# Kernel tuning notes

Hardware: AMD Instinct MI355X
Metric: run time of the kernel (lower is better)

The kernel has to match this reference:

```python
import jax, jax.numpy as jnp
import numpy as np

N_NODES = 50000
N_EDGES = 600000
D_IN = 128
D_HID = 128
NUM_LAYERS = 4


def setup_inputs() -> dict:
    key = jax.random.key(0)
    ks = jax.random.split(key, 8)
    x = jax.random.normal(ks[0], (N_NODES, D_IN), dtype=jnp.float32)
    edge_index = jax.random.randint(ks[1], (2, N_EDGES), 0, N_NODES, dtype=jnp.int32)
    s = 0.05
    # first_conv: lin_rel (weight+bias) applied to aggregated neighbors, lin_root (no bias) applied to x
    W1 = jax.random.normal(ks[2], (D_IN, D_HID), dtype=jnp.float32) * s
    b1 = jnp.zeros((D_HID,), dtype=jnp.float32)
    R1 = jax.random.normal(ks[3], (D_IN, D_HID), dtype=jnp.float32) * s
    # shared conv used for layers 2..NUM_LAYERS
    W2 = jax.random.normal(ks[4], (D_HID, D_HID), dtype=jnp.float32) * s
    b2 = jnp.zeros((D_HID,), dtype=jnp.float32)
    R2 = jax.random.normal(ks[5], (D_HID, D_HID), dtype=jnp.float32) * s
    return {"x": x, "edge_index": edge_index, "W1": W1, "b1": b1, "R1": R1,
            "W2": W2, "b2": b2, "R2": R2}


def _graph_conv(x, src, dst, W, b, R, num_nodes):
    # gather source features, scatter-max into destinations (PyG GraphConv, aggr='max')
    agg = jax.ops.segment_max(x[src], dst, num_segments=num_nodes)  # [N, d]
    agg = jnp.where(jnp.isneginf(agg), 0.0, agg)  # isolated nodes -> 0 (PyG fill)
    return agg @ W + b + x @ R  # lin_rel(agg) + lin_root(x)


def reference(x, edge_index, W1, b1, R1, W2, b2, R2):
    src, dst = edge_index[0], edge_index[1]
    n = x.shape[0]
    h = jax.nn.relu(_graph_conv(x, src, dst, W1, b1, R1, n))
    for _ in range(NUM_LAYERS - 1):  # shared weights, per original module
        h = jax.nn.relu(_graph_conv(h, src, dst, W2, b2, R2, n))
    return h
```

## Files before the change

kernel.cpp:

```cpp
#include <hip/hip_runtime.h>
#include <math.h>

static constexpr int NNODES = 50000;
static constexpr int NEDGES = 600000;
static constexpr int D = 128;
static constexpr int NPART = (NNODES + 255) / 256;

typedef __attribute__((ext_vector_type(8))) short short8;
typedef __attribute__((ext_vector_type(4))) float f32x4;

static __device__ inline unsigned short f2bf_rne(float f) {
  unsigned u = __float_as_uint(f);
  unsigned r = (u + 0x7FFFu + ((u >> 16) & 1u)) >> 16;
  return (unsigned short)r;
}
static __device__ inline float bf2f(unsigned short s) {
  return __uint_as_float(((unsigned)s) << 16);
}

__global__ __launch_bounds__(256) void split_kernel(const float* __restrict__ x,
    unsigned short* __restrict__ hi, unsigned short* __restrict__ lo, int n4) {
  int i = blockIdx.x * 256 + threadIdx.x;
  if (i >= n4) return;
  f32x4 v = *(const f32x4*)(x + (size_t)i * 4);
  ushort4 h, l;
  h.x = f2bf_rne(v[0]); l.x = f2bf_rne(v[0] - bf2f(h.x));
  h.y = f2bf_rne(v[1]); l.y = f2bf_rne(v[1] - bf2f(h.y));
  h.z = f2bf_rne(v[2]); l.z = f2bf_rne(v[2] - bf2f(h.z));
  h.w = f2bf_rne(v[3]); l.w = f2bf_rne(v[3] - bf2f(h.w));
  *(ushort4*)(hi + (size_t)i * 4) = h;
  *(ushort4*)(lo + (size_t)i * 4) = l;
}


__global__ void count_kernel(const int* __restrict__ dst, int* __restrict__ cnt, int nE) {
  int i = blockIdx.x * blockDim.x + threadIdx.x;
  if (i < nE) atomicAdd(&cnt[dst[i]], 1);
}

__global__ void scan_partial(const int* __restrict__ cnt, int* __restrict__ part, int n) {
  int i = blockIdx.x * 256 + threadIdx.x;
  int v = (i < n) ? cnt[i] : 0;
#pragma unroll
  for (int off = 32; off > 0; off >>= 1) v += __shfl_down(v, off);
  __shared__ int ws[4];
  int wid = threadIdx.x >> 6, lane = threadIdx.x & 63;
  if (lane == 0) ws[wid] = v;
  __syncthreads();
  if (threadIdx.x == 0) part[blockIdx.x] = ws[0] + ws[1] + ws[2] + ws[3];
}

__global__ void scan_root(const int* __restrict__ part, int* __restrict__ pscan,
                          int* __restrict__ rs_last, int np) {
  int i = threadIdx.x;
  int v = (i < np) ? part[i] : 0;
  int incl = v;
  int lane = i & 63, wid = i >> 6;
#pragma unroll
  for (int off = 1; off < 64; off <<= 1) {
    int t = __shfl_up(incl, off);
    if (lane >= off) incl += t;
  }
  __shared__ int ws[4];
  if (lane == 63) ws[wid] = incl;
  __syncthreads();
  int woff = 0;
  for (int w = 0; w < wid; ++w) woff += ws[w];
  if (i < np) pscan[i] = woff + incl - v;
  if (i == 0) *rs_last = ws[0] + ws[1] + ws[2] + ws[3];
}

__global__ void scan_apply(const int* __restrict__ cnt, const int* __restrict__ pscan,
                           int* __restrict__ rs, int* __restrict__ cursor, int n) {
  int i = blockIdx.x * 256 + threadIdx.x;
  int v = (i < n) ? cnt[i] : 0;
  int incl = v;
  int lane = threadIdx.x & 63, wid = threadIdx.x >> 6;
#pragma unroll
  for (int off = 1; off < 64; off <<= 1) {
    int t = __shfl_up(incl, off);
    if (lane >= off) incl += t;
  }
  __shared__ int ws[4];
  if (lane == 63) ws[wid] = incl;
  __syncthreads();
  int woff = pscan[blockIdx.x];
  for (int w = 0; w < wid; ++w) woff += ws[w];
  int ex = woff + incl - v;
  if (i < n) { rs[i] = ex; cursor[i] = ex; }
}

__global__ void fill_kernel(const int* __restrict__ src, const int* __restrict__ dst,
                            int* __restrict__ cursor, int* __restrict__ csr, int nE) {
  int i = blockIdx.x * blockDim.x + threadIdx.x;
  if (i < nE) {
    int d = dst[i];
    int p = atomicAdd(&cursor[d], 1);
    csr[p] = src[i];
  }
}

__global__ __launch_bounds__(256) void agg_kernel(const unsigned int* __restrict__ xb,
    const int* __restrict__ rs, const int* __restrict__ csr,
    unsigned int* __restrict__ aggb, int n) {
  int gw = (int)((blockIdx.x * blockDim.x + threadIdx.x) >> 6);
  int lane = threadIdx.x & 63;
  if (gw >= n) return;
  int beg = rs[gw], end = rs[gw + 1];
  float ax = -INFINITY, ay = -INFINITY;
  int j = beg;
  for (; j + 8 <= end; j += 8) {
    int s[8];
#pragma unroll
    for (int u = 0; u < 8; ++u) s[u] = csr[j + u];
    unsigned v[8];
#pragma unroll
    for (int u = 0; u < 8; ++u) v[u] = xb[(size_t)s[u] * 64 + lane];
#pragma unroll
    for (int u = 0; u < 8; ++u) {
      ax = fmaxf(ax, bf2f((unsigned short)(v[u] & 0xFFFFu)));
      ay = fmaxf(ay, bf2f((unsigned short)(v[u] >> 16)));
    }
  }
  for (; j < end; ++j) {
    unsigned v = xb[(size_t)csr[j] * 64 + lane];
    ax = fmaxf(ax, bf2f((unsigned short)(v & 0xFFFFu)));
    ay = fmaxf(ay, bf2f((unsigned short)(v >> 16)));
  }
  if (beg == end) { ax = 0.f; ay = 0.f; }
  aggb[(size_t)gw * 64 + lane] =
      (__float_as_uint(ax) >> 16) | (__float_as_uint(ay) & 0xFFFF0000u);
}

struct PackArgs {
  const float* src[4];
  unsigned short* hi[4];
  unsigned short* lo[4];
};

__global__ void pack_all(PackArgs pa) {
  int mat = blockIdx.x >> 3;
  int tid = (blockIdx.x & 7) * 256 + threadIdx.x;
  const float* Wm = pa.src[mat];
  unsigned short* hi = pa.hi[mat];
  unsigned short* lo = pa.lo[mat];
  int jb = tid >> 8;
  int ks = (tid >> 6) & 3;
  int lane = tid & 63;
  int j = jb * 16 + (lane & 15);
  int k0 = ks * 32 + (lane >> 4) * 8;
#pragma unroll
  for (int e = 0; e < 8; ++e) {
    float v = Wm[(k0 + e) * D + j];
    unsigned short h = f2bf_rne(v);
    float rem = v - bf2f(h);
    unsigned short l = f2bf_rne(rem);
    hi[tid * 8 + e] = h;
    lo[tid * 8 + e] = l;
  }
}

__global__ __launch_bounds__(256) void gemm_mfma(
    const unsigned short* __restrict__ aggb,
    const unsigned short* __restrict__ hhi, const unsigned short* __restrict__ hlo,
    const unsigned short* __restrict__ Whi, const unsigned short* __restrict__ Wlo,
    const unsigned short* __restrict__ Rhi, const unsigned short* __restrict__ Rlo,
    const float* __restrict__ bias, float* __restrict__ outf,
    unsigned short* __restrict__ ohi, unsigned short* __restrict__ olo, int nrows) {
  const int lane = threadIdx.x & 63;
  const int wv = threadIdx.x >> 6;
  const int m_lo = lane & 15;
  const int kgrp = lane >> 4;
  const int r_base = blockIdx.x * 128 + wv * 32;

  f32x4 acc[2][8];
#pragma unroll
  for (int g = 0; g < 2; ++g)
#pragma unroll
    for (int jb = 0; jb < 8; ++jb) acc[g][jb] = (f32x4)0.f;

  float bv[8];
#pragma unroll
  for (int jb = 0; jb < 8; ++jb) bv[jb] = bias[jb * 16 + m_lo];

  for (int ks = 0; ks < 4; ++ks) {
    short8 fa[2], fhh[2], fhl[2];
#pragma unroll
    for (int g = 0; g < 2; ++g) {
      int row = r_base + g * 16 + m_lo;
      if (row >= nrows) row = nrows - 1;
      const size_t ro = (size_t)row * D + ks * 32 + kgrp * 8;
      fa[g]  = *(const short8*)(aggb + ro);
      fhh[g] = *(const short8*)(hhi + ro);
      fhl[g] = *(const short8*)(hlo + ro);
    }
#pragma unroll
    for (int jb = 0; jb < 8; ++jb) {
      const int pidx = ((jb * 4 + ks) * 64 + lane) * 8;
      short8 bwhi = *(const short8*)(Whi + pidx);
      short8 bwlo = *(const short8*)(Wlo + pidx);
      short8 brhi = *(const short8*)(Rhi + pidx);
      short8 brlo = *(const short8*)(Rlo + pidx);
#pragma unroll
      for (int g = 0; g < 2; ++g) {
        acc[g][jb] = __builtin_amdgcn_mfma_f32_16x16x32_bf16(fa[g],  bwhi, acc[g][jb], 0, 0, 0);
        acc[g][jb] = __builtin_amdgcn_mfma_f32_16x16x32_bf16(fa[g],  bwlo, acc[g][jb], 0, 0, 0);
        acc[g][jb] = __builtin_amdgcn_mfma_f32_16x16x32_bf16(fhh[g], brhi, acc[g][jb], 0, 0, 0);
        acc[g][jb] = __builtin_amdgcn_mfma_f32_16x16x32_bf16(fhl[g], brhi, acc[g][jb], 0, 0, 0);
        acc[g][jb] = __builtin_amdgcn_mfma_f32_16x16x32_bf16(fhh[g], brlo, acc[g][jb], 0, 0, 0);
      }
    }
  }

#pragma unroll
  for (int g = 0; g < 2; ++g) {
#pragma unroll
    for (int jb = 0; jb < 8; ++jb) {
#pragma unroll
      for (int r = 0; r < 4; ++r) {
        int row = r_base + g * 16 + kgrp * 4 + r;
        if (row < nrows) {
          float v = fmaxf(acc[g][jb][r] + bv[jb], 0.f);
          size_t o = (size_t)row * D + jb * 16 + m_lo;
          if (outf) {
            outf[o] = v;
          } else {
            unsigned short h = f2bf_rne(v);
            ohi[o] = h;
            olo[o] = f2bf_rne(v - bf2f(h));
          }
        }
      }
    }
  }
}


extern "C" void kernel_launch(void* const* d_in, const int* in_sizes, int n_in,
                              void* d_out, int out_size, void* d_ws, size_t ws_size,
                              hipStream_t stream) {
  const float* x  = (const float*)d_in[0];
  const int*   ei = (const int*)d_in[1];
  const float* W1 = (const float*)d_in[2];
  const float* b1 = (const float*)d_in[3];
  const float* R1 = (const float*)d_in[4];
  const float* W2 = (const float*)d_in[5];
  const float* b2 = (const float*)d_in[6];
  const float* R2 = (const float*)d_in[7];
  float* out = (float*)d_out;

  const int* src = ei;
  const int* dst = ei + NEDGES;

  char* ws = (char*)d_ws;
  size_t off = 0;
  auto alloc = [&](size_t bytes) -> void* {
    off = (off + 511) & ~(size_t)511;
    void* p = ws + off;
    off += bytes;
    return p;
  };
  const size_t NF = (size_t)NNODES * D;
  unsigned short* xhi  = (unsigned short*)alloc(sizeof(short) * NF);
  unsigned short* xlo  = (unsigned short*)alloc(sizeof(short) * NF);
  unsigned short* hAhi = (unsigned short*)alloc(sizeof(short) * NF);
  unsigned short* hAlo = (unsigned short*)alloc(sizeof(short) * NF);
  unsigned short* hBhi = (unsigned short*)alloc(sizeof(short) * NF);
  unsigned short* hBlo = (unsigned short*)alloc(sizeof(short) * NF);
  unsigned short* aggb = (unsigned short*)alloc(sizeof(short) * NF);
  int* cnt    = (int*)alloc(sizeof(int) * NNODES);
  int* rs     = (int*)alloc(sizeof(int) * (NNODES + 1));
  int* cursor = (int*)alloc(sizeof(int) * NNODES);
  int* csr    = (int*)alloc(sizeof(int) * NEDGES);
  int* part   = (int*)alloc(sizeof(int) * NPART);
  int* pscan  = (int*)alloc(sizeof(int) * NPART);
  const int PACKN = 2048 * 8;
  unsigned short* w1hi = (unsigned short*)alloc(sizeof(short) * PACKN);
  unsigned short* w1lo = (unsigned short*)alloc(sizeof(short) * PACKN);
  unsigned short* r1hi = (unsigned short*)alloc(sizeof(short) * PACKN);
  unsigned short* r1lo = (unsigned short*)alloc(sizeof(short) * PACKN);
  unsigned short* w2hi = (unsigned short*)alloc(sizeof(short) * PACKN);
  unsigned short* w2lo = (unsigned short*)alloc(sizeof(short) * PACKN);
  unsigned short* r2hi = (unsigned short*)alloc(sizeof(short) * PACKN);
  unsigned short* r2lo = (unsigned short*)alloc(sizeof(short) * PACKN);

  split_kernel<<<(int)(NF / 4 + 255) / 256, 256, 0, stream>>>(x, xhi, xlo, (int)(NF / 4));

  PackArgs pa;
  pa.src[0] = W1; pa.hi[0] = w1hi; pa.lo[0] = w1lo;
  pa.src[1] = R1; pa.hi[1] = r1hi; pa.lo[1] = r1lo;
  pa.src[2] = W2; pa.hi[2] = w2hi; pa.lo[2] = w2lo;
  pa.src[3] = R2; pa.hi[3] = r2hi; pa.lo[3] = r2lo;
  pack_all<<<32, 256, 0, stream>>>(pa);

  hipMemsetAsync(cnt, 0, sizeof(int) * NNODES, stream);
  count_kernel<<<(NEDGES + 255) / 256, 256, 0, stream>>>(dst, cnt, NEDGES);
  scan_partial<<<NPART, 256, 0, stream>>>(cnt, part, NNODES);
  scan_root<<<1, 256, 0, stream>>>(part, pscan, &rs[NNODES], NPART);
  scan_apply<<<NPART, 256, 0, stream>>>(cnt, pscan, rs, cursor, NNODES);
  fill_kernel<<<(NEDGES + 255) / 256, 256, 0, stream>>>(src, dst, cursor, csr, NEDGES);

  const int gemm_grid = (NNODES + 127) / 128;

  auto layer = [&](const unsigned short* hhi, const unsigned short* hlo,
                   const unsigned short* whi, const unsigned short* wlo,
                   const unsigned short* rhi, const unsigned short* rlo,
                   const float* b, float* outf, unsigned short* ohi, unsigned short* olo) {
    agg_kernel<<<(NNODES + 3) / 4, 256, 0, stream>>>(
        (const unsigned int*)hhi, rs, csr, (unsigned int*)aggb, NNODES);
    gemm_mfma<<<gemm_grid, 256, 0, stream>>>(aggb, hhi, hlo, whi, wlo, rhi, rlo,
                                             b, outf, ohi, olo, NNODES);
  };

  layer(xhi,  xlo,  w1hi, w1lo, r1hi, r1lo, b1, nullptr, hAhi, hAlo);
  layer(hAhi, hAlo, w2hi, w2lo, r2hi, r2lo, b2, nullptr, hBhi, hBlo);
  layer(hBhi, hBlo, w2hi, w2lo, r2hi, r2lo, b2, nullptr, hAhi, hAlo);
  layer(hAhi, hAlo, w2hi, w2lo, r2hi, r2lo, b2, out, nullptr, nullptr);
}
```

Baseline: 415.3 us.

## Fuse max aggregation into GEMM kernel via swizzled LDS tile

Merges the separate gather/max aggregation kernel into the MFMA GEMM kernel. Each wave aggregates its 32 rows, processing two rows at a time with interleaved neighbor loads, and writes the packed bf16 results into an XOR-swizzled LDS tile that feeds the A-operand. This removes the global aggb write and re-read and one launch per layer. In exchange, the aggregation runs with only 391 blocks (one per 128 rows) instead of 12500, which lowers parallelism and latency hiding for the irregular gathers. Pairing rows also wastes loads when the two degrees differ.

```diff
diff --git a/kernel.cpp b/kernel.cpp
--- a/kernel.cpp
+++ b/kernel.cpp
@@ -100,38 +100,6 @@
   }
 }
 
-__global__ __launch_bounds__(256) void agg_kernel(const unsigned int* __restrict__ xb,
-    const int* __restrict__ rs, const int* __restrict__ csr,
-    unsigned int* __restrict__ aggb, int n) {
-  int gw = (int)((blockIdx.x * blockDim.x + threadIdx.x) >> 6);
-  int lane = threadIdx.x & 63;
-  if (gw >= n) return;
-  int beg = rs[gw], end = rs[gw + 1];
-  float ax = -INFINITY, ay = -INFINITY;
-  int j = beg;
-  for (; j + 8 <= end; j += 8) {
-    int s[8];
-#pragma unroll
-    for (int u = 0; u < 8; ++u) s[u] = csr[j + u];
-    unsigned v[8];
-#pragma unroll
-    for (int u = 0; u < 8; ++u) v[u] = xb[(size_t)s[u] * 64 + lane];
-#pragma unroll
-    for (int u = 0; u < 8; ++u) {
-      ax = fmaxf(ax, bf2f((unsigned short)(v[u] & 0xFFFFu)));
-      ay = fmaxf(ay, bf2f((unsigned short)(v[u] >> 16)));
-    }
-  }
-  for (; j < end; ++j) {
-    unsigned v = xb[(size_t)csr[j] * 64 + lane];
-    ax = fmaxf(ax, bf2f((unsigned short)(v & 0xFFFFu)));
-    ay = fmaxf(ay, bf2f((unsigned short)(v >> 16)));
-  }
-  if (beg == end) { ax = 0.f; ay = 0.f; }
-  aggb[(size_t)gw * 64 + lane] =
-      (__float_as_uint(ax) >> 16) | (__float_as_uint(ay) & 0xFFFF0000u);
-}
-
 struct PackArgs {
   const float* src[4];
   unsigned short* hi[4];
@@ -160,18 +128,61 @@
   }
 }
 
-__global__ __launch_bounds__(256) void gemm_mfma(
-    const unsigned short* __restrict__ aggb,
+__global__ __launch_bounds__(256) void layer_fused(
     const unsigned short* __restrict__ hhi, const unsigned short* __restrict__ hlo,
+    const int* __restrict__ rs, const int* __restrict__ csr,
     const unsigned short* __restrict__ Whi, const unsigned short* __restrict__ Wlo,
     const unsigned short* __restrict__ Rhi, const unsigned short* __restrict__ Rlo,
     const float* __restrict__ bias, float* __restrict__ outf,
     unsigned short* __restrict__ ohi, unsigned short* __restrict__ olo, int nrows) {
+  __shared__ unsigned lds[4][2048];
   const int lane = threadIdx.x & 63;
   const int wv = threadIdx.x >> 6;
   const int m_lo = lane & 15;
-  const int kgrp = lane >> 4;
+  const int sub = lane >> 4;
   const int r_base = blockIdx.x * 128 + wv * 32;
+  const unsigned* __restrict__ xb = (const unsigned*)hhi;
+  const float NEG = __uint_as_float(0xFF800000u);
+  unsigned* ldsw = &lds[wv][0];
+
+  for (int ip = 0; ip < 16; ++ip) {
+    const int i0 = ip * 2, i1 = ip * 2 + 1;
+    int b0 = 0, e0 = 0, b1 = 0, e1 = 0;
+    { int r0 = r_base + i0; if (r0 < nrows) { b0 = rs[r0]; e0 = rs[r0 + 1]; } }
+    { int r1 = r_base + i1; if (r1 < nrows) { b1 = rs[r1]; e1 = rs[r1 + 1]; } }
+    float ax0 = NEG, ay0 = NEG, ax1 = NEG, ay1 = NEG;
+    const int c0 = (e0 > 0) ? e0 - 1 : 0;
+    const int c1 = (e1 > 0) ? e1 - 1 : 0;
+    int j0 = b0, j1 = b1;
+    while (j0 < e0 || j1 < e1) {
+      unsigned v0[8], v1[8];
+#pragma unroll
+      for (int u = 0; u < 8; ++u) {
+        int q0 = j0 + u, q1 = j1 + u;
+        int s0 = csr[q0 <= c0 ? q0 : c0];
+        int s1 = csr[q1 <= c1 ? q1 : c1];
+        v0[u] = xb[(size_t)s0 * 64 + lane];
+        v1[u] = xb[(size_t)s1 * 64 + lane];
+      }
+#pragma unroll
+      for (int u = 0; u < 8; ++u) {
+        unsigned w0 = (j0 + u < e0) ? v0[u] : 0xFF80FF80u;
+        unsigned w1 = (j1 + u < e1) ? v1[u] : 0xFF80FF80u;
+        ax0 = fmaxf(ax0, __uint_as_float(w0 << 16));
+        ay0 = fmaxf(ay0, __uint_as_float(w0 & 0xFFFF0000u));
+        ax1 = fmaxf(ax1, __uint_as_float(w1 << 16));
+        ay1 = fmaxf(ay1, __uint_as_float(w1 & 0xFFFF0000u));
+      }
+      j0 += 8; j1 += 8;
+    }
+    if (b0 == e0) { ax0 = 0.f; ay0 = 0.f; }
+    if (b1 == e1) { ax1 = 0.f; ay1 = 0.f; }
+    unsigned p0 = (__float_as_uint(ax0) >> 16) | (__float_as_uint(ay0) & 0xFFFF0000u);
+    unsigned p1 = (__float_as_uint(ax1) >> 16) | (__float_as_uint(ay1) & 0xFFFF0000u);
+    ldsw[(i0 * 256 + ((lane * 4) ^ ((i0 & 7) << 4))) >> 2] = p0;
+    ldsw[(i1 * 256 + ((lane * 4) ^ ((i1 & 7) << 4))) >> 2] = p1;
+  }
+  __syncthreads();
 
   f32x4 acc[2][8];
 #pragma unroll
@@ -183,14 +194,16 @@
 #pragma unroll
   for (int jb = 0; jb < 8; ++jb) bv[jb] = bias[jb * 16 + m_lo];
 
+  const char* ldsc = (const char*)&lds[wv][0];
   for (int ks = 0; ks < 4; ++ks) {
     short8 fa[2], fhh[2], fhl[2];
 #pragma unroll
     for (int g = 0; g < 2; ++g) {
-      int row = r_base + g * 16 + m_lo;
-      if (row >= nrows) row = nrows - 1;
-      const size_t ro = (size_t)row * D + ks * 32 + kgrp * 8;
-      fa[g]  = *(const short8*)(aggb + ro);
+      int ri = g * 16 + m_lo;
+      int bofs = ri * 256 + (((ks * 64) + (sub * 16)) ^ ((ri & 7) << 4));
+      fa[g] = *(const short8*)(ldsc + bofs);
+      int row = r_base + g * 16 + m_lo; if (row >= nrows) row = nrows - 1;
+      const size_t ro = (size_t)row * D + ks * 32 + sub * 8;
       fhh[g] = *(const short8*)(hhi + ro);
       fhl[g] = *(const short8*)(hlo + ro);
     }
@@ -218,7 +231,7 @@
     for (int jb = 0; jb < 8; ++jb) {
 #pragma unroll
       for (int r = 0; r < 4; ++r) {
-        int row = r_base + g * 16 + kgrp * 4 + r;
+        int row = r_base + g * 16 + sub * 4 + r;
         if (row < nrows) {
           float v = fmaxf(acc[g][jb][r] + bv[jb], 0.f);
           size_t o = (size_t)row * D + jb * 16 + m_lo;
@@ -267,7 +280,6 @@
   unsigned short* hAlo = (unsigned short*)alloc(sizeof(short) * NF);
   unsigned short* hBhi = (unsigned short*)alloc(sizeof(short) * NF);
   unsigned short* hBlo = (unsigned short*)alloc(sizeof(short) * NF);
-  unsigned short* aggb = (unsigned short*)alloc(sizeof(short) * NF);
   int* cnt    = (int*)alloc(sizeof(int) * NNODES);
   int* rs     = (int*)alloc(sizeof(int) * (NNODES + 1));
   int* cursor = (int*)alloc(sizeof(int) * NNODES);
@@ -300,16 +312,14 @@
   scan_apply<<<NPART, 256, 0, stream>>>(cnt, pscan, rs, cursor, NNODES);
   fill_kernel<<<(NEDGES + 255) / 256, 256, 0, stream>>>(src, dst, cursor, csr, NEDGES);
 
-  const int gemm_grid = (NNODES + 127) / 128;
+  const int grid = (NNODES + 127) / 128;
 
   auto layer = [&](const unsigned short* hhi, const unsigned short* hlo,
                    const unsigned short* whi, const unsigned short* wlo,
                    const unsigned short* rhi, const unsigned short* rlo,
                    const float* b, float* outf, unsigned short* ohi, unsigned short* olo) {
-    agg_kernel<<<(NNODES + 3) / 4, 256, 0, stream>>>(
-        (const unsigned int*)hhi, rs, csr, (unsigned int*)aggb, NNODES);
-    gemm_mfma<<<gemm_grid, 256, 0, stream>>>(aggb, hhi, hlo, whi, wlo, rhi, rlo,
-                                             b, outf, ohi, olo, NNODES);
+    layer_fused<<<grid, 256, 0, stream>>>(hhi, hlo, rs, csr, whi, wlo, rhi, rlo,
+                                          b, outf, ohi, olo, NNODES);
   };
 
   layer(xhi,  xlo,  w1hi, w1lo, r1hi, r1lo, b1, nullptr, hAhi, hAlo);
```

After: 424.1 us. 1.02x slower.

## Fuse neighbor max-aggregation into the MFMA GEMM via LDS staging

Applied to the files above, without the earlier changes.

Merges the per-layer aggregation kernel and the GEMM kernel into one kernel. Each wave first aggregates 16 rows serially, writing the bf16 max results into swizzled LDS, then runs the MFMA GEMM reading the aggregated operand from LDS instead of a global buffer. This removes the global round-trip of the aggregation buffer and one launch per layer. In exchange each wave handles 16 rows instead of 32 (less weight reuse per block) and processes its 16 gathers sequentially, which may reduce gather parallelism and latency hiding.

```diff
diff --git a/kernel.cpp b/kernel.cpp
--- a/kernel.cpp
+++ b/kernel.cpp
@@ -100,38 +100,6 @@
   }
 }
 
-__global__ __launch_bounds__(256) void agg_kernel(const unsigned int* __restrict__ xb,
-    const int* __restrict__ rs, const int* __restrict__ csr,
-    unsigned int* __restrict__ aggb, int n) {
-  int gw = (int)((blockIdx.x * blockDim.x + threadIdx.x) >> 6);
-  int lane = threadIdx.x & 63;
-  if (gw >= n) return;
-  int beg = rs[gw], end = rs[gw + 1];
-  float ax = -INFINITY, ay = -INFINITY;
-  int j = beg;
-  for (; j + 8 <= end; j += 8) {
-    int s[8];
-#pragma unroll
-    for (int u = 0; u < 8; ++u) s[u] = csr[j + u];
-    unsigned v[8];
-#pragma unroll
-    for (int u = 0; u < 8; ++u) v[u] = xb[(size_t)s[u] * 64 + lane];
-#pragma unroll
-    for (int u = 0; u < 8; ++u) {
-      ax = fmaxf(ax, bf2f((unsigned short)(v[u] & 0xFFFFu)));
-      ay = fmaxf(ay, bf2f((unsigned short)(v[u] >> 16)));
-    }
-  }
-  for (; j < end; ++j) {
-    unsigned v = xb[(size_t)csr[j] * 64 + lane];
-    ax = fmaxf(ax, bf2f((unsigned short)(v & 0xFFFFu)));
-    ay = fmaxf(ay, bf2f((unsigned short)(v >> 16)));
-  }
-  if (beg == end) { ax = 0.f; ay = 0.f; }
-  aggb[(size_t)gw * 64 + lane] =
-      (__float_as_uint(ax) >> 16) | (__float_as_uint(ay) & 0xFFFF0000u);
-}
-
 struct PackArgs {
   const float* src[4];
   unsigned short* hi[4];
@@ -160,39 +128,72 @@
   }
 }
 
-__global__ __launch_bounds__(256) void gemm_mfma(
-    const unsigned short* __restrict__ aggb,
+__global__ __launch_bounds__(256) void layer_fused(
     const unsigned short* __restrict__ hhi, const unsigned short* __restrict__ hlo,
+    const int* __restrict__ rs, const int* __restrict__ csr,
     const unsigned short* __restrict__ Whi, const unsigned short* __restrict__ Wlo,
     const unsigned short* __restrict__ Rhi, const unsigned short* __restrict__ Rlo,
     const float* __restrict__ bias, float* __restrict__ outf,
     unsigned short* __restrict__ ohi, unsigned short* __restrict__ olo, int nrows) {
+  __shared__ unsigned lds[4][1024];
   const int lane = threadIdx.x & 63;
   const int wv = threadIdx.x >> 6;
   const int m_lo = lane & 15;
-  const int kgrp = lane >> 4;
-  const int r_base = blockIdx.x * 128 + wv * 32;
-
-  f32x4 acc[2][8];
-#pragma unroll
-  for (int g = 0; g < 2; ++g)
-#pragma unroll
-    for (int jb = 0; jb < 8; ++jb) acc[g][jb] = (f32x4)0.f;
+  const int sub = lane >> 4;
+  const int r_base = blockIdx.x * 64 + wv * 16;
+  const unsigned* __restrict__ xb = (const unsigned*)hhi;
+  const float NEG = __uint_as_float(0xFF800000u);
+  unsigned* ldsw = &lds[wv][0];
+
+  for (int i = 0; i < 16; ++i) {
+    int row = r_base + i;
+    int beg = 0, end = 0;
+    if (row < nrows) { beg = rs[row]; end = rs[row + 1]; }
+    float ax = NEG, ay = NEG;
+    int j = beg;
+    for (; j + 8 <= end; j += 8) {
+      int s[8];
+#pragma unroll
+      for (int u = 0; u < 8; ++u) s[u] = csr[j + u];
+      unsigned v[8];
+#pragma unroll
+      for (int u = 0; u < 8; ++u) v[u] = xb[(size_t)s[u] * 64 + lane];
+#pragma unroll
+      for (int u = 0; u < 8; ++u) {
+        ax = fmaxf(ax, __uint_as_float(v[u] << 16));
+        ay = fmaxf(ay, __uint_as_float(v[u] & 0xFFFF0000u));
+      }
+    }
+    for (; j < end; ++j) {
+      unsigned v = xb[(size_t)csr[j] * 64 + lane];
+      ax = fmaxf(ax, __uint_as_float(v << 16));
+      ay = fmaxf(ay, __uint_as_float(v & 0xFFFF0000u));
+    }
+    if (beg == end) { ax = 0.f; ay = 0.f; }
+    unsigned p = (__float_as_uint(ax) >> 16) | (__float_as_uint(ay) & 0xFFFF0000u);
+    ldsw[(i * 256 + ((lane * 4) ^ ((i & 7) << 4))) >> 2] = p;
+  }
+  __syncthreads();
+
+  f32x4 acc[8];
+#pragma unroll
+  for (int jb = 0; jb < 8; ++jb) acc[jb] = (f32x4)0.f;
 
   float bv[8];
 #pragma unroll
   for (int jb = 0; jb < 8; ++jb) bv[jb] = bias[jb * 16 + m_lo];
 
+  const char* ldsc = (const char*)&lds[wv][0];
   for (int ks = 0; ks < 4; ++ks) {
-    short8 fa[2], fhh[2], fhl[2];
-#pragma unroll
-    for (int g = 0; g < 2; ++g) {
-      int row = r_base + g * 16 + m_lo;
-      if (row >= nrows) row = nrows - 1;
-      const size_t ro = (size_t)row * D + ks * 32 + kgrp * 8;
-      fa[g]  = *(const short8*)(aggb + ro);
-      fhh[g] = *(const short8*)(hhi + ro);
-      fhl[g] = *(const short8*)(hlo + ro);
+    short8 fa, fhh, fhl;
+    {
+      int ri = m_lo;
+      int bofs = ri * 256 + (((ks * 64) + (sub * 16)) ^ ((ri & 7) << 4));
+      fa = *(const short8*)(ldsc + bofs);
+      int row = r_base + m_lo; if (row >= nrows) row = nrows - 1;
+      const size_t ro = (size_t)row * D + ks * 32 + sub * 8;
+      fhh = *(const short8*)(hhi + ro);
+      fhl = *(const short8*)(hlo + ro);
     }
 #pragma unroll
     for (int jb = 0; jb < 8; ++jb) {
@@ -201,34 +202,28 @@
       short8 bwlo = *(const short8*)(Wlo + pidx);
       short8 brhi = *(const short8*)(Rhi + pidx);
       short8 brlo = *(const short8*)(Rlo + pidx);
-#pragma unroll
-      for (int g = 0; g < 2; ++g) {
-        acc[g][jb] = __builtin_amdgcn_mfma_f32_16x16x32_bf16(fa[g],  bwhi, acc[g][jb], 0, 0, 0);
-        acc[g][jb] = __builtin_amdgcn_mfma_f32_16x16x32_bf16(fa[g],  bwlo, acc[g][jb], 0, 0, 0);
-        acc[g][jb] = __builtin_amdgcn_mfma_f32_16x16x32_bf16(fhh[g], brhi, acc[g][jb], 0, 0, 0);
-        acc[g][jb] = __builtin_amdgcn_mfma_f32_16x16x32_bf16(fhl[g], brhi, acc[g][jb], 0, 0, 0);
-        acc[g][jb] = __builtin_amdgcn_mfma_f32_16x16x32_bf16(fhh[g], brlo, acc[g][jb], 0, 0, 0);
-      }
-    }
-  }
-
-#pragma unroll
-  for (int g = 0; g < 2; ++g) {
-#pragma unroll
-    for (int jb = 0; jb < 8; ++jb) {
-#pragma unroll
-      for (int r = 0; r < 4; ++r) {
-        int row = r_base + g * 16 + kgrp * 4 + r;
-        if (row < nrows) {
-          float v = fmaxf(acc[g][jb][r] + bv[jb], 0.f);
-          size_t o = (size_t)row * D + jb * 16 + m_lo;
-          if (outf) {
-            outf[o] = v;
-          } else {
-            unsigned short h = f2bf_rne(v);
-            ohi[o] = h;
-            olo[o] = f2bf_rne(v - bf2f(h));
-          }
+      acc[jb] = __builtin_amdgcn_mfma_f32_16x16x32_bf16(fa,  bwhi, acc[jb], 0, 0, 0);
+      acc[jb] = __builtin_amdgcn_mfma_f32_16x16x32_bf16(fa,  bwlo, acc[jb], 0, 0, 0);
+      acc[jb] = __builtin_amdgcn_mfma_f32_16x16x32_bf16(fhh, brhi, acc[jb], 0, 0, 0);
+      acc[jb] = __builtin_amdgcn_mfma_f32_16x16x32_bf16(fhl, brhi, acc[jb], 0, 0, 0);
+      acc[jb] = __builtin_amdgcn_mfma_f32_16x16x32_bf16(fhh, brlo, acc[jb], 0, 0, 0);
+    }
+  }
+
+#pragma unroll
+  for (int jb = 0; jb < 8; ++jb) {
+#pragma unroll
+    for (int r = 0; r < 4; ++r) {
+      int row = r_base + sub * 4 + r;
+      if (row < nrows) {
+        float v = fmaxf(acc[jb][r] + bv[jb], 0.f);
+        size_t o = (size_t)row * D + jb * 16 + m_lo;
+        if (outf) {
+          outf[o] = v;
+        } else {
+          unsigned short h = f2bf_rne(v);
+          ohi[o] = h;
+          olo[o] = f2bf_rne(v - bf2f(h));
         }
       }
     }
@@ -267,7 +262,6 @@
   unsigned short* hAlo = (unsigned short*)alloc(sizeof(short) * NF);
   unsigned short* hBhi = (unsigned short*)alloc(sizeof(short) * NF);
   unsigned short* hBlo = (unsigned short*)alloc(sizeof(short) * NF);
-  unsigned short* aggb = (unsigned short*)alloc(sizeof(short) * NF);
   int* cnt    = (int*)alloc(sizeof(int) * NNODES);
   int* rs     = (int*)alloc(sizeof(int) * (NNODES + 1));
   int* cursor = (int*)alloc(sizeof(int) * NNODES);
@@ -300,16 +294,14 @@
   scan_apply<<<NPART, 256, 0, stream>>>(cnt, pscan, rs, cursor, NNODES);
   fill_kernel<<<(NEDGES + 255) / 256, 256, 0, stream>>>(src, dst, cursor, csr, NEDGES);
 
-  const int gemm_grid = (NNODES + 127) / 128;
+  const int grid = (NNODES + 63) / 64;
 
   auto layer = [&](const unsigned short* hhi, const unsigned short* hlo,
                    const unsigned short* whi, const unsigned short* wlo,
                    const unsigned short* rhi, const unsigned short* rlo,
                    const float* b, float* outf, unsigned short* ohi, unsigned short* olo) {
-    agg_kernel<<<(NNODES + 3) / 4, 256, 0, stream>>>(
-        (const unsigned int*)hhi, rs, csr, (unsigned int*)aggb, NNODES);
-    gemm_mfma<<<gemm_grid, 256, 0, stream>>>(aggb, hhi, hlo, whi, wlo, rhi, rlo,
-                                             b, outf, ohi, olo, NNODES);
+    layer_fused<<<grid, 256, 0, stream>>>(hhi, hlo, rs, csr, whi, wlo, rhi, rlo,
+                                          b, outf, ohi, olo, NNODES);
   };
 
   layer(xhi,  xlo,  w1hi, w1lo, r1hi, r1lo, b1, nullptr, hAhi, hAlo);
```

After: 473.2 us. +13.9%, slower.
